# Kernel tuning notes

Measured on AMD Instinct MI355X. Metric: run time of the kernel, lower is better.

## Reference

```python
import jax, jax.numpy as jnp
import numpy as np

B, D, L = 16, 64, 1280
H = 8            # nhead
WIN = 5          # window_size (divides L exactly)
DFF = 128        # dim_feedforward
EPS = 1e-5


def _layernorm(x, g, b):
    mu = jnp.mean(x, axis=-1, keepdims=True)
    var = jnp.mean(jnp.square(x - mu), axis=-1, keepdims=True)
    return (x - mu) * jax.lax.rsqrt(var + EPS) * g + b


def _mha(x, w_in, b_in, w_out, b_out):
    # x: (Bx, Lx, D). torch nn.MultiheadAttention, batch_first, eval mode.
    Bx, Lx, Dm = x.shape
    hd = Dm // H
    qkv = x @ w_in.T + b_in                      # (Bx, Lx, 3D)
    q, k, v = jnp.split(qkv, 3, axis=-1)
    q = q.reshape(Bx, Lx, H, hd)
    k = k.reshape(Bx, Lx, H, hd)
    v = v.reshape(Bx, Lx, H, hd)
    scale = 1.0 / jnp.sqrt(jnp.asarray(hd, x.dtype))
    scores = jnp.einsum('bqhd,bkhd->bhqk', q, k) * scale
    att = jax.nn.softmax(scores, axis=-1)
    out = jnp.einsum('bhqk,bkhd->bqhd', att, v).reshape(Bx, Lx, Dm)
    return out @ w_out.T + b_out


def setup_inputs() -> dict:
    key = jax.random.key(0)
    ks = jax.random.split(key, 16)
    s = 0.05
    return {
        'x': jax.random.normal(ks[0], (B, D, L), dtype=jnp.float32),
        # local attention params
        'lw_in': jax.random.normal(ks[1], (3 * D, D), dtype=jnp.float32) * s,
        'lb_in': jnp.zeros((3 * D,), jnp.float32),
        'lw_out': jax.random.normal(ks[2], (D, D), dtype=jnp.float32) * s,
        'lb_out': jnp.zeros((D,), jnp.float32),
        # global attention params
        'gw_in': jax.random.normal(ks[3], (3 * D, D), dtype=jnp.float32) * s,
        'gb_in': jnp.zeros((3 * D,), jnp.float32),
        'gw_out': jax.random.normal(ks[4], (D, D), dtype=jnp.float32) * s,
        'gb_out': jnp.zeros((D,), jnp.float32),
        # gating weight (init 0.5 like the module)
        'local_weight': jnp.full((D,), 0.5, jnp.float32),
        # layer norms
        'g1': jnp.ones((D,), jnp.float32), 'b1': jnp.zeros((D,), jnp.float32),
        'g2': jnp.ones((D,), jnp.float32), 'b2': jnp.zeros((D,), jnp.float32),
        'g3': jnp.ones((D,), jnp.float32), 'b3': jnp.zeros((D,), jnp.float32),
        # FFN
        'w1': jax.random.normal(ks[5], (DFF, D), dtype=jnp.float32) * s,
        'bf1': jnp.zeros((DFF,), jnp.float32),
        'w2': jax.random.normal(ks[6], (D, DFF), dtype=jnp.float32) * s,
        'bf2': jnp.zeros((D,), jnp.float32),
    }


def reference(x, lw_in, lb_in, lw_out, lb_out, gw_in, gb_in, gw_out, gb_out,
              local_weight, g1, b1, g2, b2, g3, b3, w1, bf1, w2, bf2):
    xt = jnp.transpose(x, (0, 2, 1))              # (B, L, D)
    residual = xt
    nW = L // WIN
    xw = xt.reshape(B * nW, WIN, D)
    local_out = _mha(xw, lw_in, lb_in, lw_out, lb_out).reshape(B, L, D)
    local_out = _layernorm(local_out + residual, g1, b1)
    # global attention
    global_out = _mha(xt, gw_in, gb_in, gw_out, gb_out)
    global_out = _layernorm(global_out + residual, g2, b2)
    # gated channel fusion
    alpha = jax.nn.sigmoid(local_weight)[None, None, :]
    fused = alpha * local_out + (1.0 - alpha) * global_out
    # FFN (dropout is identity in eval mode)
    ffn_out = jax.nn.relu(fused @ w1.T + bf1) @ w2.T + bf2
    out = _layernorm(ffn_out + fused, g3, b3)
    return jnp.transpose(out, (0, 2, 1))          # (B, D, L)
```

## Files before the change

kernel.cpp:

```cpp
#include <hip/hip_runtime.h>
#include <math.h>

typedef short bf16x8 __attribute__((ext_vector_type(8)));
typedef float f32x4 __attribute__((ext_vector_type(4)));
typedef unsigned short u16;
typedef unsigned int u32;

#define RFL(x) __builtin_amdgcn_readfirstlane(x)

static __device__ __forceinline__ float bf2f(u16 s) {
  union { u32 u; float f; } c; c.u = ((u32)s) << 16; return c.f;
}
static __device__ __forceinline__ u16 f2bf(float f) {
  union { float f; u32 u; } c; c.f = f;
  u32 u = c.u + 0x7fffu + ((c.u >> 16) & 1u);
  return (u16)(u >> 16);
}
static __device__ __forceinline__ u32 pk2(float lo, float hi) {
  u32 r;
  asm("v_cvt_pk_bf16_f32 %0, %1, %2" : "=v"(r) : "v"(lo), "v"(hi));
  return r;
}
static __device__ __forceinline__ f32x4 MF(bf16x8 a, bf16x8 b, f32x4 c) {
  return __builtin_amdgcn_mfma_f32_16x16x32_bf16(a, b, c, 0, 0, 0);
}


__global__ __launch_bounds__(256) void prep_kernel(
    const float* __restrict__ x,
    const float* __restrict__ lw_in, const float* __restrict__ gw_in,
    const float* __restrict__ lw_out, const float* __restrict__ gw_out,
    const float* __restrict__ w1, const float* __restrict__ w2,
    u16* __restrict__ XT, u16* __restrict__ Wqkv,
    u16* __restrict__ Wlout, u16* __restrict__ Wgout,
    u16* __restrict__ W1b, u16* __restrict__ W2b) {
  const int t = threadIdx.x;
  if (blockIdx.x < 320) {
    __shared__ __align__(16) float xs[64][68];
    const int b = blockIdx.x / 20, l0 = (blockIdx.x % 20) * 64;
    for (int i = t; i < 4096; i += 256) {
      const int d = i >> 6, tok = i & 63;
      xs[tok][d] = x[(b * 64 + d) * 1280 + l0 + tok];
    }
    __syncthreads();
    for (int i = t; i < 512; i += 256) {
      const int tok = i >> 3, c8 = (i & 7) * 8;
      union { bf16x8 v; u32 u[4]; } o;
      const float* src = &xs[tok][c8];
      o.u[0] = pk2(src[0], src[1]); o.u[1] = pk2(src[2], src[3]);
      o.u[2] = pk2(src[4], src[5]); o.u[3] = pk2(src[6], src[7]);
      *(bf16x8*)(XT + (b * 1280 + l0 + tok) * 64 + c8) = o.v;
    }
  } else {
    const int wb = blockIdx.x - 320;
    for (int f = wb * 256 + t; f < 49152; f += 24 * 256) {
      if (f < 12288)      Wqkv[f] = f2bf(lw_in[f]);
      else if (f < 24576) Wqkv[f] = f2bf(gw_in[f - 12288]);
      else if (f < 28672) Wlout[f - 24576] = f2bf(lw_out[f - 24576]);
      else if (f < 32768) Wgout[f - 28672] = f2bf(gw_out[f - 28672]);
      else if (f < 40960) W1b[f - 32768] = f2bf(w1[f - 32768]);
      else                W2b[f - 40960] = f2bf(w2[f - 40960]);
    }
  }
}

__global__ __launch_bounds__(256) void qkv_gemm(
    const u16* __restrict__ XT, const u16* __restrict__ Wqkv,
    const float* __restrict__ lb_in, const float* __restrict__ gb_in,
    u16* __restrict__ QKV) {
  const int t = threadIdx.x;
  const int lane = t & 63, w = RFL(t >> 6);
  const int lr = lane & 15, lg = lane >> 4;
  const int m0 = blockIdx.x * 64 + (w & 1) * 32;
  const int n0 = blockIdx.y * 96 + (w >> 1) * 48;
  bf16x8 a[2][2], bb[3][2];
#pragma unroll
  for (int mt = 0; mt < 2; ++mt)
#pragma unroll
    for (int ks = 0; ks < 2; ++ks)
      a[mt][ks] = *(const bf16x8*)(XT + (m0 + mt * 16 + lr) * 64 + ks * 32 + lg * 8);
#pragma unroll
  for (int nt = 0; nt < 3; ++nt)
#pragma unroll
    for (int ks = 0; ks < 2; ++ks)
      bb[nt][ks] = *(const bf16x8*)(Wqkv + (n0 + nt * 16 + lr) * 64 + ks * 32 + lg * 8);
  f32x4 acc[2][3];
#pragma unroll
  for (int mt = 0; mt < 2; ++mt)
#pragma unroll
    for (int nt = 0; nt < 3; ++nt) {
      f32x4 z = {0.f, 0.f, 0.f, 0.f};
      acc[mt][nt] = z;
#pragma unroll
      for (int ks = 0; ks < 2; ++ks)
        acc[mt][nt] = MF(a[mt][ks], bb[nt][ks], acc[mt][nt]);
    }
#pragma unroll
  for (int nt = 0; nt < 3; ++nt) {
    const int col = n0 + nt * 16 + lr;
    const float bias = (col < 192) ? lb_in[col] : gb_in[col - 192];
    const float scale = (col < 64) ? 0.35355339059327373f
                      : ((col >= 192 && col < 256) ? 0.51010407600615432f : 1.f);
#pragma unroll
    for (int mt = 0; mt < 2; ++mt)
#pragma unroll
      for (int r = 0; r < 4; ++r) {
        const int row = m0 + mt * 16 + 4 * lg + r;
        QKV[row * 384 + col] = f2bf((acc[mt][nt][r] + bias) * scale);
      }
  }
}

__global__ __launch_bounds__(256) void latt(const u16* __restrict__ QKV,
                                            u16* __restrict__ AOl) {
  const int g = blockIdx.x * 256 + threadIdx.x;
  const int qi = g % 5, h = (g / 5) & 7, wi = (g / 40) & 255, b = g / 10240;
  const int row = b * 1280 + wi * 5 + qi;
  float q[8];
  {
    bf16x8 qv = *(const bf16x8*)(QKV + row * 384 + h * 8);
#pragma unroll
    for (int d = 0; d < 8; ++d) q[d] = bf2f((u16)qv[d]);
  }
  float p[5], sum = 0.f;
#pragma unroll
  for (int j = 0; j < 5; ++j) {
    const int krow = b * 1280 + wi * 5 + j;
    bf16x8 kv = *(const bf16x8*)(QKV + krow * 384 + 64 + h * 8);
    float s = 0.f;
#pragma unroll
    for (int d = 0; d < 8; ++d) s = fmaf(q[d], bf2f((u16)kv[d]), s);
    p[j] = __expf(s); sum += p[j];
  }
  const float inv = 1.f / sum;
  float o[8] = {0, 0, 0, 0, 0, 0, 0, 0};
#pragma unroll
  for (int j = 0; j < 5; ++j) {
    const int vrow = b * 1280 + wi * 5 + j;
    bf16x8 vv = *(const bf16x8*)(QKV + vrow * 384 + 128 + h * 8);
#pragma unroll
    for (int d = 0; d < 8; ++d) o[d] = fmaf(p[j], bf2f((u16)vv[d]), o[d]);
  }
  union { bf16x8 v; u32 u[4]; } ov;
  ov.u[0] = pk2(o[0] * inv, o[1] * inv); ov.u[1] = pk2(o[2] * inv, o[3] * inv);
  ov.u[2] = pk2(o[4] * inv, o[5] * inv); ov.u[3] = pk2(o[6] * inv, o[7] * inv);
  *(bf16x8*)(AOl + row * 64 + h * 8) = ov.v;
}

__global__ __launch_bounds__(512) void gatt(const u16* __restrict__ QKV,
                                            u16* __restrict__ AOg) {
  __shared__ __align__(16) u16 Klds[1280 * 8];
  __shared__ __align__(16) u16 VT[9 * 1320];
  const int t = threadIdx.x;
  const int b = blockIdx.y >> 3, h = blockIdx.y & 7;
  for (int l = t; l < 1280; l += 512) {
    const int src = (b * 1280 + l) * 384 + h * 8;
    bf16x8 kv = *(const bf16x8*)(QKV + src + 256);
    bf16x8 vv = *(const bf16x8*)(QKV + src + 320);
    const int k5 = l & 31;
    const int pos = (l & ~31) + (((k5 >> 2) & 1) << 4) + (k5 & 3) + ((k5 >> 3) << 2);
    *(bf16x8*)(Klds + pos * 8) = kv;
#pragma unroll
    for (int d = 0; d < 8; ++d) VT[d * 1320 + l] = (u16)vv[d];
  }
  for (int l = t; l < 1320; l += 512) VT[8 * 1320 + l] = 0x3F80;
  __syncthreads();
  const int lane = t & 63, w = RFL(t >> 6);
  const int c = lane & 15, lg = lane >> 4;
  const int q0 = blockIdx.x * 128 + w * 16;
  const int qrow = b * 1280 + q0 + c;
  const bf16x8 qv = *(const bf16x8*)(QKV + qrow * 384 + 192 + h * 8);
  const bf16x8 qz = {0, 0, 0, 0, 0, 0, 0, 0};
  const bf16x8 qf = (lg == 0) ? qv : qz;
  const u16* kp = Klds + c * 8;
  const int vrow = (c < 8) ? c : 8;
  const u16* vp = VT + vrow * 1320 + lg * 8;
  f32x4 oacc = {0.f, 0.f, 0.f, 0.f};
#pragma unroll 4
  for (int jt = 0; jt < 40; ++jt) {
    bf16x8 kf0 = *(const bf16x8*)kp;
    bf16x8 kf1 = *(const bf16x8*)(kp + 128);
    f32x4 z = {0.f, 0.f, 0.f, 0.f};
    f32x4 s0 = MF(kf0, qf, z);
    f32x4 s1 = MF(kf1, qf, z);
    const float p0 = __builtin_amdgcn_exp2f(s0[0]);
    const float p1 = __builtin_amdgcn_exp2f(s0[1]);
    const float p2 = __builtin_amdgcn_exp2f(s0[2]);
    const float p3 = __builtin_amdgcn_exp2f(s0[3]);
    const float p4 = __builtin_amdgcn_exp2f(s1[0]);
    const float p5 = __builtin_amdgcn_exp2f(s1[1]);
    const float p6 = __builtin_amdgcn_exp2f(s1[2]);
    const float p7 = __builtin_amdgcn_exp2f(s1[3]);
    union { u32 u[4]; bf16x8 v; } pb;
    pb.u[0] = pk2(p0, p1);
    pb.u[1] = pk2(p2, p3);
    pb.u[2] = pk2(p4, p5);
    pb.u[3] = pk2(p6, p7);
    bf16x8 vf = *(const bf16x8*)vp;
    oacc = MF(vf, pb.v, oacc);
    kp += 256; vp += 32;
  }
  const float ssum = __shfl(oacc[0], 32 + c);
  const float inv = 1.f / ssum;
  if (lg < 2) {
    const int base = qrow * 64 + h * 8 + lg * 4;
    *(u32*)(AOg + base) = pk2(oacc[0] * inv, oacc[1] * inv);
    *(u32*)(AOg + base + 2) = pk2(oacc[2] * inv, oacc[3] * inv);
  }
}

__global__ __launch_bounds__(256) void tail_kernel(
    const u16* __restrict__ AOl, const u16* __restrict__ AOg,
    const u16* __restrict__ Wlout, const u16* __restrict__ Wgout,
    const u16* __restrict__ W1b, const u16* __restrict__ W2b,
    const float* __restrict__ lb_out, const float* __restrict__ gb_out,
    const float* __restrict__ lwt,
    const float* __restrict__ g1, const float* __restrict__ b1,
    const float* __restrict__ g2, const float* __restrict__ b2,
    const float* __restrict__ g3, const float* __restrict__ b3,
    const float* __restrict__ bf1, const float* __restrict__ bf2,
    const float* __restrict__ x, float* __restrict__ out) {
  __shared__ __align__(16) float xso[64][68];
  __shared__ __align__(16) u16 Ft[64 * 64];
  __shared__ __align__(16) u16 Ht[64 * 128];
  const int t = threadIdx.x;
  const int b = blockIdx.y, l0 = blockIdx.x * 64;
  for (int i = t; i < 4096; i += 256) {
    const int d = i >> 6, tok = i & 63;
    xso[d][tok] = x[(b * 64 + d) * 1280 + l0 + tok];
  }
  __syncthreads();
  const int lane = t & 63, w = RFL(t >> 6);
  const int lr = lane & 15, lg = lane >> 4;
  const int tb = w * 16;
  const int grow = b * 1280 + l0 + tb;

  f32x4 accl[4], accg[4];
#pragma unroll
  for (int nt = 0; nt < 4; ++nt) { f32x4 z = {0,0,0,0}; accl[nt] = z; accg[nt] = z; }
#pragma unroll
  for (int ks = 0; ks < 2; ++ks) {
    bf16x8 al = *(const bf16x8*)(AOl + (grow + lr) * 64 + ks * 32 + lg * 8);
    bf16x8 ag = *(const bf16x8*)(AOg + (grow + lr) * 64 + ks * 32 + lg * 8);
#pragma unroll
    for (int nt = 0; nt < 4; ++nt) {
      bf16x8 bl = *(const bf16x8*)(Wlout + (nt * 16 + lr) * 64 + ks * 32 + lg * 8);
      bf16x8 bg = *(const bf16x8*)(Wgout + (nt * 16 + lr) * 64 + ks * 32 + lg * 8);
      accl[nt] = MF(al, bl, accl[nt]);
      accg[nt] = MF(ag, bg, accg[nt]);
    }
  }
#pragma unroll
  for (int nt = 0; nt < 4; ++nt) {
    const int col = nt * 16 + lr;
    const float bl = lb_out[col], bg = gb_out[col];
    f32x4 xr = *(const f32x4*)&xso[col][tb + lg * 4];
#pragma unroll
    for (int r = 0; r < 4; ++r) {
      accl[nt][r] += bl + xr[r];
      accg[nt][r] += bg + xr[r];
    }
  }
  auto LN = [&](f32x4* a, const float* gam, const float* bet) {
    float gv[4], bv[4];
#pragma unroll
    for (int nt = 0; nt < 4; ++nt) { gv[nt] = gam[nt * 16 + lr]; bv[nt] = bet[nt * 16 + lr]; }
#pragma unroll
    for (int r = 0; r < 4; ++r) {
      float s = a[0][r] + a[1][r] + a[2][r] + a[3][r];
      s += __shfl_xor(s, 1); s += __shfl_xor(s, 2);
      s += __shfl_xor(s, 4); s += __shfl_xor(s, 8);
      const float mu = s * 0.015625f;
      float q = 0.f;
#pragma unroll
      for (int nt = 0; nt < 4; ++nt) { const float cv = a[nt][r] - mu; q = fmaf(cv, cv, q); }
      q += __shfl_xor(q, 1); q += __shfl_xor(q, 2);
      q += __shfl_xor(q, 4); q += __shfl_xor(q, 8);
      const float rsq = rsqrtf(q * 0.015625f + 1e-5f);
#pragma unroll
      for (int nt = 0; nt < 4; ++nt)
        a[nt][r] = (a[nt][r] - mu) * rsq * gv[nt] + bv[nt];
    }
  };
  LN(accl, g1, b1);
  LN(accg, g2, b2);
  f32x4 fus[4];
#pragma unroll
  for (int nt = 0; nt < 4; ++nt) {
    const int col = nt * 16 + lr;
    const float al_ = 1.f / (1.f + __expf(-lwt[col]));
#pragma unroll
    for (int r = 0; r < 4; ++r)
      fus[nt][r] = al_ * accl[nt][r] + (1.f - al_) * accg[nt][r];
  }
#pragma unroll
  for (int nt = 0; nt < 4; ++nt)
#pragma unroll
    for (int r = 0; r < 4; ++r) {
      const int ltok = tb + lg * 4 + r;
      const int byteoff = ((ltok * 64 + nt * 16 + lr) * 2) ^ ((ltok & 7) << 4);
      *(u16*)((char*)Ft + byteoff) = f2bf(fus[nt][r]);
    }
  asm volatile("" ::: "memory");
  __syncthreads();
  f32x4 hcc[8];
#pragma unroll
  for (int nt = 0; nt < 8; ++nt) { f32x4 z = {0,0,0,0}; hcc[nt] = z; }
#pragma unroll
  for (int ks = 0; ks < 2; ++ks) {
    const int ltokA = tb + lr;
    const int abyte = (ltokA * 128 + ks * 64 + lg * 16) ^ ((ltokA & 7) << 4);
    bf16x8 af = *(const bf16x8*)((char*)Ft + abyte);
#pragma unroll
    for (int nt = 0; nt < 8; ++nt) {
      bf16x8 bw = *(const bf16x8*)(W1b + (nt * 16 + lr) * 64 + ks * 32 + lg * 8);
      hcc[nt] = MF(af, bw, hcc[nt]);
    }
  }
#pragma unroll
  for (int nt = 0; nt < 8; ++nt) {
    const int f = nt * 16 + lr;
    const float bbv = bf1[f];
#pragma unroll
    for (int r = 0; r < 4; ++r) {
      const float v = fmaxf(hcc[nt][r] + bbv, 0.f);
      const int ltok = tb + lg * 4 + r;
      const int byteoff = ((ltok * 256 + f * 2)) ^ ((ltok & 7) << 4);
      *(u16*)((char*)Ht + byteoff) = f2bf(v);
    }
  }
  asm volatile("" ::: "memory");
  f32x4 occ[4];
#pragma unroll
  for (int nt = 0; nt < 4; ++nt) { f32x4 z = {0,0,0,0}; occ[nt] = z; }
#pragma unroll
  for (int ks = 0; ks < 4; ++ks) {
    const int ltokA = tb + lr;
    const int abyte = (ltokA * 256 + ks * 64 + lg * 16) ^ ((ltokA & 7) << 4);
    bf16x8 af = *(const bf16x8*)((char*)Ht + abyte);
#pragma unroll
    for (int nt = 0; nt < 4; ++nt) {
      bf16x8 bw = *(const bf16x8*)(W2b + (nt * 16 + lr) * 128 + ks * 32 + lg * 8);
      occ[nt] = MF(af, bw, occ[nt]);
    }
  }
#pragma unroll
  for (int nt = 0; nt < 4; ++nt) {
    const float bb2 = bf2[nt * 16 + lr];
#pragma unroll
    for (int r = 0; r < 4; ++r) occ[nt][r] += bb2 + fus[nt][r];
  }
  LN(occ, g3, b3);
#pragma unroll
  for (int nt = 0; nt < 4; ++nt)
#pragma unroll
    for (int r = 0; r < 4; ++r)
      xso[nt * 16 + lr][tb + lg * 4 + r] = occ[nt][r];
  __syncthreads();
  for (int i = t; i < 4096; i += 256) {
    const int d = i >> 6, tok = i & 63;
    out[(b * 64 + d) * 1280 + l0 + tok] = xso[d][tok];
  }
}

extern "C" void kernel_launch(void* const* d_in, const int* in_sizes, int n_in,
                              void* d_out, int out_size, void* d_ws,
                              size_t ws_size, hipStream_t stream) {
  const float* x      = (const float*)d_in[0];
  const float* lw_in  = (const float*)d_in[1];
  const float* lb_in  = (const float*)d_in[2];
  const float* lw_out = (const float*)d_in[3];
  const float* lb_out = (const float*)d_in[4];
  const float* gw_in  = (const float*)d_in[5];
  const float* gb_in  = (const float*)d_in[6];
  const float* gw_out = (const float*)d_in[7];
  const float* gb_out = (const float*)d_in[8];
  const float* lwt    = (const float*)d_in[9];
  const float* g1 = (const float*)d_in[10]; const float* b1 = (const float*)d_in[11];
  const float* g2 = (const float*)d_in[12]; const float* b2 = (const float*)d_in[13];
  const float* g3 = (const float*)d_in[14]; const float* b3 = (const float*)d_in[15];
  const float* w1 = (const float*)d_in[16]; const float* bf1 = (const float*)d_in[17];
  const float* w2 = (const float*)d_in[18]; const float* bf2 = (const float*)d_in[19];
  float* out = (float*)d_out;

  u16* XT    = (u16*)d_ws;
  u16* QKV   = XT + 1310720;
  u16* AOl   = QKV + 7864320;
  u16* AOg   = AOl + 1310720;
  u16* Wqkv  = AOg + 1310720;
  u16* Wlout = Wqkv + 24576;
  u16* Wgout = Wlout + 4096;
  u16* W1b   = Wgout + 4096;
  u16* W2b   = W1b + 8192;

  dim3 blk(256);
  prep_kernel<<<dim3(344), blk, 0, stream>>>(x, lw_in, gw_in, lw_out, gw_out,
                                             w1, w2, XT, Wqkv, Wlout, Wgout, W1b, W2b);
  qkv_gemm<<<dim3(320, 4), blk, 0, stream>>>(XT, Wqkv, lb_in, gb_in, QKV);
  latt<<<dim3(640), blk, 0, stream>>>(QKV, AOl);
  gatt<<<dim3(10, 128), dim3(512), 0, stream>>>(QKV, AOg);
  tail_kernel<<<dim3(20, 16), blk, 0, stream>>>(
      AOl, AOg, Wlout, Wgout, W1b, W2b, lb_out, gb_out, lwt,
      g1, b1, g2, b2, g3, b3, bf1, bf2, x, out);
}
```

Baseline: 79.57 us.

## Fuse prep into QKV GEMM, merge attention kernels, shrink tail blocks

Fuses the x transpose/bf16 conversion and in_proj weight conversion straight into the QKV GEMM, which now stages x through swizzled LDS and converts fp32 weights in registers. The local attention, global attention and remaining weight conversion become one launch by partitioning the grid. The tail kernel moves to 64-thread blocks over 16 tokens for more blocks. Together this drops two launches and the XT/Wqkv workspace round trip, at the cost of each QKV block re-reading and re-converting the full fp32 weights, and a more heterogeneous grid in the merged attention kernel.

```diff
diff --git a/kernel.cpp b/kernel.cpp
--- a/kernel.cpp
+++ b/kernel.cpp
@@ -26,69 +26,61 @@
 }
 
 
-__global__ __launch_bounds__(256) void prep_kernel(
-    const float* __restrict__ x,
-    const float* __restrict__ lw_in, const float* __restrict__ gw_in,
-    const float* __restrict__ lw_out, const float* __restrict__ gw_out,
-    const float* __restrict__ w1, const float* __restrict__ w2,
-    u16* __restrict__ XT, u16* __restrict__ Wqkv,
-    u16* __restrict__ Wlout, u16* __restrict__ Wgout,
-    u16* __restrict__ W1b, u16* __restrict__ W2b) {
+__global__ __launch_bounds__(256) void qkvx(
+    const float* __restrict__ x, const float* __restrict__ lw_in,
+    const float* __restrict__ gw_in, const float* __restrict__ lb_in,
+    const float* __restrict__ gb_in, u16* __restrict__ QKV) {
+  __shared__ __align__(16) float xs[32][68];
+  __shared__ __align__(16) u16 XTs[32 * 64];
   const int t = threadIdx.x;
-  if (blockIdx.x < 320) {
-    __shared__ __align__(16) float xs[64][68];
-    const int b = blockIdx.x / 20, l0 = (blockIdx.x % 20) * 64;
-    for (int i = t; i < 4096; i += 256) {
-      const int d = i >> 6, tok = i & 63;
-      xs[tok][d] = x[(b * 64 + d) * 1280 + l0 + tok];
-    }
-    __syncthreads();
-    for (int i = t; i < 512; i += 256) {
-      const int tok = i >> 3, c8 = (i & 7) * 8;
-      union { bf16x8 v; u32 u[4]; } o;
-      const float* src = &xs[tok][c8];
-      o.u[0] = pk2(src[0], src[1]); o.u[1] = pk2(src[2], src[3]);
-      o.u[2] = pk2(src[4], src[5]); o.u[3] = pk2(src[6], src[7]);
-      *(bf16x8*)(XT + (b * 1280 + l0 + tok) * 64 + c8) = o.v;
-    }
-  } else {
-    const int wb = blockIdx.x - 320;
-    for (int f = wb * 256 + t; f < 49152; f += 24 * 256) {
-      if (f < 12288)      Wqkv[f] = f2bf(lw_in[f]);
-      else if (f < 24576) Wqkv[f] = f2bf(gw_in[f - 12288]);
-      else if (f < 28672) Wlout[f - 24576] = f2bf(lw_out[f - 24576]);
-      else if (f < 32768) Wgout[f - 28672] = f2bf(gw_out[f - 28672]);
-      else if (f < 40960) W1b[f - 32768] = f2bf(w1[f - 32768]);
-      else                W2b[f - 40960] = f2bf(w2[f - 40960]);
-    }
-  }
-}
-
-__global__ __launch_bounds__(256) void qkv_gemm(
-    const u16* __restrict__ XT, const u16* __restrict__ Wqkv,
-    const float* __restrict__ lb_in, const float* __restrict__ gb_in,
-    u16* __restrict__ QKV) {
-  const int t = threadIdx.x;
+  const int b = blockIdx.x / 40, l0 = (blockIdx.x % 40) * 32;
+  for (int i = t; i < 2048; i += 256) {
+    const int d = i >> 5, tok = i & 31;
+    xs[tok][d] = x[(b * 64 + d) * 1280 + l0 + tok];
+  }
+  __syncthreads();
+  {
+    const int tok = t >> 3, c8 = (t & 7) * 8;
+    union { bf16x8 v; u32 u[4]; } o;
+    const float* src = &xs[tok][c8];
+    o.u[0] = pk2(src[0], src[1]); o.u[1] = pk2(src[2], src[3]);
+    o.u[2] = pk2(src[4], src[5]); o.u[3] = pk2(src[6], src[7]);
+    const int byteoff = (tok * 128 + c8 * 2) ^ ((tok & 7) << 4);
+    *(bf16x8*)((char*)XTs + byteoff) = o.v;
+  }
+  __syncthreads();
   const int lane = t & 63, w = RFL(t >> 6);
   const int lr = lane & 15, lg = lane >> 4;
-  const int m0 = blockIdx.x * 64 + (w & 1) * 32;
-  const int n0 = blockIdx.y * 96 + (w >> 1) * 48;
-  bf16x8 a[2][2], bb[3][2];
+  const int n0 = w * 96;
+  bf16x8 a[2][2];
 #pragma unroll
   for (int mt = 0; mt < 2; ++mt)
 #pragma unroll
-    for (int ks = 0; ks < 2; ++ks)
-      a[mt][ks] = *(const bf16x8*)(XT + (m0 + mt * 16 + lr) * 64 + ks * 32 + lg * 8);
-#pragma unroll
-  for (int nt = 0; nt < 3; ++nt)
-#pragma unroll
-    for (int ks = 0; ks < 2; ++ks)
-      bb[nt][ks] = *(const bf16x8*)(Wqkv + (n0 + nt * 16 + lr) * 64 + ks * 32 + lg * 8);
-  f32x4 acc[2][3];
+    for (int ks = 0; ks < 2; ++ks) {
+      const int row = mt * 16 + lr;
+      const int abyte = (row * 128 + ks * 64 + lg * 16) ^ ((row & 7) << 4);
+      a[mt][ks] = *(const bf16x8*)((char*)XTs + abyte);
+    }
+  const float* W32 = (n0 < 192) ? lw_in : gw_in;
+  const int nb = (n0 < 192) ? n0 : n0 - 192;
+  bf16x8 bb[6][2];
+#pragma unroll
+  for (int nt = 0; nt < 6; ++nt)
+#pragma unroll
+    for (int ks = 0; ks < 2; ++ks) {
+      const float* src = W32 + (nb + nt * 16 + lr) * 64 + ks * 32 + lg * 8;
+      const float4 f0 = *(const float4*)src;
+      const float4 f1 = *(const float4*)(src + 4);
+      union { bf16x8 v; u32 u[4]; } o;
+      o.u[0] = pk2(f0.x, f0.y); o.u[1] = pk2(f0.z, f0.w);
+      o.u[2] = pk2(f1.x, f1.y); o.u[3] = pk2(f1.z, f1.w);
+      bb[nt][ks] = o.v;
+    }
+  f32x4 acc[2][6];
 #pragma unroll
   for (int mt = 0; mt < 2; ++mt)
 #pragma unroll
-    for (int nt = 0; nt < 3; ++nt) {
+    for (int nt = 0; nt < 6; ++nt) {
       f32x4 z = {0.f, 0.f, 0.f, 0.f};
       acc[mt][nt] = z;
 #pragma unroll
@@ -96,7 +88,7 @@
         acc[mt][nt] = MF(a[mt][ks], bb[nt][ks], acc[mt][nt]);
     }
 #pragma unroll
-  for (int nt = 0; nt < 3; ++nt) {
+  for (int nt = 0; nt < 6; ++nt) {
     const int col = n0 + nt * 16 + lr;
     const float bias = (col < 192) ? lb_in[col] : gb_in[col - 192];
     const float scale = (col < 64) ? 0.35355339059327373f
@@ -105,111 +97,123 @@
     for (int mt = 0; mt < 2; ++mt)
 #pragma unroll
       for (int r = 0; r < 4; ++r) {
-        const int row = m0 + mt * 16 + 4 * lg + r;
+        const int row = b * 1280 + l0 + mt * 16 + 4 * lg + r;
         QKV[row * 384 + col] = f2bf((acc[mt][nt][r] + bias) * scale);
       }
   }
 }
 
-__global__ __launch_bounds__(256) void latt(const u16* __restrict__ QKV,
-                                            u16* __restrict__ AOl) {
-  const int g = blockIdx.x * 256 + threadIdx.x;
-  const int qi = g % 5, h = (g / 5) & 7, wi = (g / 40) & 255, b = g / 10240;
-  const int row = b * 1280 + wi * 5 + qi;
-  float q[8];
-  {
-    bf16x8 qv = *(const bf16x8*)(QKV + row * 384 + h * 8);
-#pragma unroll
-    for (int d = 0; d < 8; ++d) q[d] = bf2f((u16)qv[d]);
-  }
-  float p[5], sum = 0.f;
-#pragma unroll
-  for (int j = 0; j < 5; ++j) {
-    const int krow = b * 1280 + wi * 5 + j;
-    bf16x8 kv = *(const bf16x8*)(QKV + krow * 384 + 64 + h * 8);
-    float s = 0.f;
-#pragma unroll
-    for (int d = 0; d < 8; ++d) s = fmaf(q[d], bf2f((u16)kv[d]), s);
-    p[j] = __expf(s); sum += p[j];
-  }
-  const float inv = 1.f / sum;
-  float o[8] = {0, 0, 0, 0, 0, 0, 0, 0};
-#pragma unroll
-  for (int j = 0; j < 5; ++j) {
-    const int vrow = b * 1280 + wi * 5 + j;
-    bf16x8 vv = *(const bf16x8*)(QKV + vrow * 384 + 128 + h * 8);
-#pragma unroll
-    for (int d = 0; d < 8; ++d) o[d] = fmaf(p[j], bf2f((u16)vv[d]), o[d]);
-  }
-  union { bf16x8 v; u32 u[4]; } ov;
-  ov.u[0] = pk2(o[0] * inv, o[1] * inv); ov.u[1] = pk2(o[2] * inv, o[3] * inv);
-  ov.u[2] = pk2(o[4] * inv, o[5] * inv); ov.u[3] = pk2(o[6] * inv, o[7] * inv);
-  *(bf16x8*)(AOl + row * 64 + h * 8) = ov.v;
-}
-
-__global__ __launch_bounds__(512) void gatt(const u16* __restrict__ QKV,
-                                            u16* __restrict__ AOg) {
+__global__ __launch_bounds__(512) void attn(
+    const u16* __restrict__ QKV, u16* __restrict__ AOl, u16* __restrict__ AOg,
+    const float* __restrict__ lw_out, const float* __restrict__ gw_out,
+    const float* __restrict__ w1, const float* __restrict__ w2,
+    u16* __restrict__ Wlout, u16* __restrict__ Wgout,
+    u16* __restrict__ W1b, u16* __restrict__ W2b) {
   __shared__ __align__(16) u16 Klds[1280 * 8];
   __shared__ __align__(16) u16 VT[9 * 1320];
   const int t = threadIdx.x;
-  const int b = blockIdx.y >> 3, h = blockIdx.y & 7;
-  for (int l = t; l < 1280; l += 512) {
-    const int src = (b * 1280 + l) * 384 + h * 8;
-    bf16x8 kv = *(const bf16x8*)(QKV + src + 256);
-    bf16x8 vv = *(const bf16x8*)(QKV + src + 320);
-    const int k5 = l & 31;
-    const int pos = (l & ~31) + (((k5 >> 2) & 1) << 4) + (k5 & 3) + ((k5 >> 3) << 2);
-    *(bf16x8*)(Klds + pos * 8) = kv;
-#pragma unroll
-    for (int d = 0; d < 8; ++d) VT[d * 1320 + l] = (u16)vv[d];
-  }
-  for (int l = t; l < 1320; l += 512) VT[8 * 1320 + l] = 0x3F80;
-  __syncthreads();
-  const int lane = t & 63, w = RFL(t >> 6);
-  const int c = lane & 15, lg = lane >> 4;
-  const int q0 = blockIdx.x * 128 + w * 16;
-  const int qrow = b * 1280 + q0 + c;
-  const bf16x8 qv = *(const bf16x8*)(QKV + qrow * 384 + 192 + h * 8);
-  const bf16x8 qz = {0, 0, 0, 0, 0, 0, 0, 0};
-  const bf16x8 qf = (lg == 0) ? qv : qz;
-  const u16* kp = Klds + c * 8;
-  const int vrow = (c < 8) ? c : 8;
-  const u16* vp = VT + vrow * 1320 + lg * 8;
-  f32x4 oacc = {0.f, 0.f, 0.f, 0.f};
+  if (blockIdx.x < 10) {
+    const int b = blockIdx.y >> 3, h = blockIdx.y & 7;
+    for (int l = t; l < 1280; l += 512) {
+      const int src = (b * 1280 + l) * 384 + h * 8;
+      bf16x8 kv = *(const bf16x8*)(QKV + src + 256);
+      bf16x8 vv = *(const bf16x8*)(QKV + src + 320);
+      const int k5 = l & 31;
+      const int pos = (l & ~31) + (((k5 >> 2) & 1) << 4) + (k5 & 3) + ((k5 >> 3) << 2);
+      *(bf16x8*)(Klds + pos * 8) = kv;
+#pragma unroll
+      for (int d = 0; d < 8; ++d) VT[d * 1320 + l] = (u16)vv[d];
+    }
+    for (int l = t; l < 1320; l += 512) VT[8 * 1320 + l] = 0x3F80;
+    __syncthreads();
+    const int lane = t & 63, w = RFL(t >> 6);
+    const int c = lane & 15, lg = lane >> 4;
+    const int q0 = blockIdx.x * 128 + w * 16;
+    const int qrow = b * 1280 + q0 + c;
+    const bf16x8 qv = *(const bf16x8*)(QKV + qrow * 384 + 192 + h * 8);
+    const bf16x8 qz = {0, 0, 0, 0, 0, 0, 0, 0};
+    const bf16x8 qf = (lg == 0) ? qv : qz;
+    const u16* kp = Klds + c * 8;
+    const int vrow = (c < 8) ? c : 8;
+    const u16* vp = VT + vrow * 1320 + lg * 8;
+    f32x4 oacc = {0.f, 0.f, 0.f, 0.f};
 #pragma unroll 4
-  for (int jt = 0; jt < 40; ++jt) {
-    bf16x8 kf0 = *(const bf16x8*)kp;
-    bf16x8 kf1 = *(const bf16x8*)(kp + 128);
-    f32x4 z = {0.f, 0.f, 0.f, 0.f};
-    f32x4 s0 = MF(kf0, qf, z);
-    f32x4 s1 = MF(kf1, qf, z);
-    const float p0 = __builtin_amdgcn_exp2f(s0[0]);
-    const float p1 = __builtin_amdgcn_exp2f(s0[1]);
-    const float p2 = __builtin_amdgcn_exp2f(s0[2]);
-    const float p3 = __builtin_amdgcn_exp2f(s0[3]);
-    const float p4 = __builtin_amdgcn_exp2f(s1[0]);
-    const float p5 = __builtin_amdgcn_exp2f(s1[1]);
-    const float p6 = __builtin_amdgcn_exp2f(s1[2]);
-    const float p7 = __builtin_amdgcn_exp2f(s1[3]);
-    union { u32 u[4]; bf16x8 v; } pb;
-    pb.u[0] = pk2(p0, p1);
-    pb.u[1] = pk2(p2, p3);
-    pb.u[2] = pk2(p4, p5);
-    pb.u[3] = pk2(p6, p7);
-    bf16x8 vf = *(const bf16x8*)vp;
-    oacc = MF(vf, pb.v, oacc);
-    kp += 256; vp += 32;
-  }
-  const float ssum = __shfl(oacc[0], 32 + c);
-  const float inv = 1.f / ssum;
-  if (lg < 2) {
-    const int base = qrow * 64 + h * 8 + lg * 4;
-    *(u32*)(AOg + base) = pk2(oacc[0] * inv, oacc[1] * inv);
-    *(u32*)(AOg + base + 2) = pk2(oacc[2] * inv, oacc[3] * inv);
-  }
-}
-
-__global__ __launch_bounds__(256) void tail_kernel(
+    for (int jt = 0; jt < 40; ++jt) {
+      bf16x8 kf0 = *(const bf16x8*)kp;
+      bf16x8 kf1 = *(const bf16x8*)(kp + 128);
+      f32x4 z = {0.f, 0.f, 0.f, 0.f};
+      f32x4 s0 = MF(kf0, qf, z);
+      f32x4 s1 = MF(kf1, qf, z);
+      const float p0 = __builtin_amdgcn_exp2f(s0[0]);
+      const float p1 = __builtin_amdgcn_exp2f(s0[1]);
+      const float p2 = __builtin_amdgcn_exp2f(s0[2]);
+      const float p3 = __builtin_amdgcn_exp2f(s0[3]);
+      const float p4 = __builtin_amdgcn_exp2f(s1[0]);
+      const float p5 = __builtin_amdgcn_exp2f(s1[1]);
+      const float p6 = __builtin_amdgcn_exp2f(s1[2]);
+      const float p7 = __builtin_amdgcn_exp2f(s1[3]);
+      union { u32 u[4]; bf16x8 v; } pb;
+      pb.u[0] = pk2(p0, p1);
+      pb.u[1] = pk2(p2, p3);
+      pb.u[2] = pk2(p4, p5);
+      pb.u[3] = pk2(p6, p7);
+      bf16x8 vf = *(const bf16x8*)vp;
+      oacc = MF(vf, pb.v, oacc);
+      kp += 256; vp += 32;
+    }
+    const float ssum = __shfl(oacc[0], 32 + c);
+    const float inv = 1.f / ssum;
+    if (lg < 2) {
+      const int base = qrow * 64 + h * 8 + lg * 4;
+      *(u32*)(AOg + base) = pk2(oacc[0] * inv, oacc[1] * inv);
+      *(u32*)(AOg + base + 2) = pk2(oacc[2] * inv, oacc[3] * inv);
+    }
+    return;
+  }
+  const int lid = (blockIdx.x - 10) * 128 + blockIdx.y;
+  if (lid < 320) {
+    const int g = lid * 512 + t;
+    const int qi = g % 5, h = (g / 5) & 7, wi = (g / 40) & 255, b = g / 10240;
+    const int row = b * 1280 + wi * 5 + qi;
+    float q[8];
+    {
+      bf16x8 qv = *(const bf16x8*)(QKV + row * 384 + h * 8);
+#pragma unroll
+      for (int d = 0; d < 8; ++d) q[d] = bf2f((u16)qv[d]);
+    }
+    float p[5], sum = 0.f;
+#pragma unroll
+    for (int j = 0; j < 5; ++j) {
+      const int krow = b * 1280 + wi * 5 + j;
+      bf16x8 kv = *(const bf16x8*)(QKV + krow * 384 + 64 + h * 8);
+      float s = 0.f;
+#pragma unroll
+      for (int d = 0; d < 8; ++d) s = fmaf(q[d], bf2f((u16)kv[d]), s);
+      p[j] = __expf(s); sum += p[j];
+    }
+    const float inv = 1.f / sum;
+    float o[8] = {0, 0, 0, 0, 0, 0, 0, 0};
+#pragma unroll
+    for (int j = 0; j < 5; ++j) {
+      const int vrow = b * 1280 + wi * 5 + j;
+      bf16x8 vv = *(const bf16x8*)(QKV + vrow * 384 + 128 + h * 8);
+#pragma unroll
+      for (int d = 0; d < 8; ++d) o[d] = fmaf(p[j], bf2f((u16)vv[d]), o[d]);
+    }
+    union { bf16x8 v; u32 u[4]; } ov;
+    ov.u[0] = pk2(o[0] * inv, o[1] * inv); ov.u[1] = pk2(o[2] * inv, o[3] * inv);
+    ov.u[2] = pk2(o[4] * inv, o[5] * inv); ov.u[3] = pk2(o[6] * inv, o[7] * inv);
+    *(bf16x8*)(AOl + row * 64 + h * 8) = ov.v;
+  } else {
+    const int f = (lid - 320) * 512 + t;
+    if (f < 4096)       Wlout[f] = f2bf(lw_out[f]);
+    else if (f < 8192)  Wgout[f - 4096] = f2bf(gw_out[f - 4096]);
+    else if (f < 16384) W1b[f - 8192] = f2bf(w1[f - 8192]);
+    else if (f < 24576) W2b[f - 16384] = f2bf(w2[f - 16384]);
+  }
+}
+
+__global__ __launch_bounds__(64) void tail_kernel(
     const u16* __restrict__ AOl, const u16* __restrict__ AOg,
     const u16* __restrict__ Wlout, const u16* __restrict__ Wgout,
     const u16* __restrict__ W1b, const u16* __restrict__ W2b,
@@ -220,20 +224,18 @@
     const float* __restrict__ g3, const float* __restrict__ b3,
     const float* __restrict__ bf1, const float* __restrict__ bf2,
     const float* __restrict__ x, float* __restrict__ out) {
-  __shared__ __align__(16) float xso[64][68];
-  __shared__ __align__(16) u16 Ft[64 * 64];
-  __shared__ __align__(16) u16 Ht[64 * 128];
+  __shared__ __align__(16) float xso[64][20];
+  __shared__ __align__(16) u16 Ft[16 * 64];
+  __shared__ __align__(16) u16 Ht[16 * 128];
   const int t = threadIdx.x;
-  const int b = blockIdx.y, l0 = blockIdx.x * 64;
-  for (int i = t; i < 4096; i += 256) {
-    const int d = i >> 6, tok = i & 63;
+  const int b = blockIdx.y, l0 = blockIdx.x * 16;
+  for (int i = t; i < 1024; i += 64) {
+    const int d = i >> 4, tok = i & 15;
     xso[d][tok] = x[(b * 64 + d) * 1280 + l0 + tok];
   }
   __syncthreads();
-  const int lane = t & 63, w = RFL(t >> 6);
-  const int lr = lane & 15, lg = lane >> 4;
-  const int tb = w * 16;
-  const int grow = b * 1280 + l0 + tb;
+  const int lr = t & 15, lg = (t & 63) >> 4;
+  const int grow = b * 1280 + l0;
 
   f32x4 accl[4], accg[4];
 #pragma unroll
@@ -254,7 +256,7 @@
   for (int nt = 0; nt < 4; ++nt) {
     const int col = nt * 16 + lr;
     const float bl = lb_out[col], bg = gb_out[col];
-    f32x4 xr = *(const f32x4*)&xso[col][tb + lg * 4];
+    f32x4 xr = *(const f32x4*)&xso[col][lg * 4];
 #pragma unroll
     for (int r = 0; r < 4; ++r) {
       accl[nt][r] += bl + xr[r];
@@ -297,8 +299,8 @@
   for (int nt = 0; nt < 4; ++nt)
 #pragma unroll
     for (int r = 0; r < 4; ++r) {
-      const int ltok = tb + lg * 4 + r;
-      const int byteoff = ((ltok * 64 + nt * 16 + lr) * 2) ^ ((ltok & 7) << 4);
+      const int ltok = lg * 4 + r;
+      const int byteoff = (ltok * 128 + (nt * 16 + lr) * 2) ^ ((ltok & 7) << 4);
       *(u16*)((char*)Ft + byteoff) = f2bf(fus[nt][r]);
     }
   asm volatile("" ::: "memory");
@@ -308,8 +310,7 @@
   for (int nt = 0; nt < 8; ++nt) { f32x4 z = {0,0,0,0}; hcc[nt] = z; }
 #pragma unroll
   for (int ks = 0; ks < 2; ++ks) {
-    const int ltokA = tb + lr;
-    const int abyte = (ltokA * 128 + ks * 64 + lg * 16) ^ ((ltokA & 7) << 4);
+    const int abyte = (lr * 128 + ks * 64 + lg * 16) ^ ((lr & 7) << 4);
     bf16x8 af = *(const bf16x8*)((char*)Ft + abyte);
 #pragma unroll
     for (int nt = 0; nt < 8; ++nt) {
@@ -324,8 +325,8 @@
 #pragma unroll
     for (int r = 0; r < 4; ++r) {
       const float v = fmaxf(hcc[nt][r] + bbv, 0.f);
-      const int ltok = tb + lg * 4 + r;
-      const int byteoff = ((ltok * 256 + f * 2)) ^ ((ltok & 7) << 4);
+      const int ltok = lg * 4 + r;
+      const int byteoff = (ltok * 256 + f * 2) ^ ((ltok & 7) << 4);
       *(u16*)((char*)Ht + byteoff) = f2bf(v);
     }
   }
@@ -335,8 +336,7 @@
   for (int nt = 0; nt < 4; ++nt) { f32x4 z = {0,0,0,0}; occ[nt] = z; }
 #pragma unroll
   for (int ks = 0; ks < 4; ++ks) {
-    const int ltokA = tb + lr;
-    const int abyte = (ltokA * 256 + ks * 64 + lg * 16) ^ ((ltokA & 7) << 4);
+    const int abyte = (lr * 256 + ks * 64 + lg * 16) ^ ((lr & 7) << 4);
     bf16x8 af = *(const bf16x8*)((char*)Ht + abyte);
 #pragma unroll
     for (int nt = 0; nt < 4; ++nt) {
@@ -355,10 +355,10 @@
   for (int nt = 0; nt < 4; ++nt)
 #pragma unroll
     for (int r = 0; r < 4; ++r)
-      xso[nt * 16 + lr][tb + lg * 4 + r] = occ[nt][r];
+      xso[nt * 16 + lr][lg * 4 + r] = occ[nt][r];
   __syncthreads();
-  for (int i = t; i < 4096; i += 256) {
-    const int d = i >> 6, tok = i & 63;
+  for (int i = t; i < 1024; i += 64) {
+    const int d = i >> 4, tok = i & 15;
     out[(b * 64 + d) * 1280 + l0 + tok] = xso[d][tok];
   }
 }
@@ -383,23 +383,18 @@
   const float* w2 = (const float*)d_in[18]; const float* bf2 = (const float*)d_in[19];
   float* out = (float*)d_out;
 
-  u16* XT    = (u16*)d_ws;
-  u16* QKV   = XT + 1310720;
+  u16* QKV   = (u16*)d_ws;
   u16* AOl   = QKV + 7864320;
   u16* AOg   = AOl + 1310720;
-  u16* Wqkv  = AOg + 1310720;
-  u16* Wlout = Wqkv + 24576;
+  u16* Wlout = AOg + 1310720;
   u16* Wgout = Wlout + 4096;
   u16* W1b   = Wgout + 4096;
   u16* W2b   = W1b + 8192;
 
-  dim3 blk(256);
-  prep_kernel<<<dim3(344), blk, 0, stream>>>(x, lw_in, gw_in, lw_out, gw_out,
-                                             w1, w2, XT, Wqkv, Wlout, Wgout, W1b, W2b);
-  qkv_gemm<<<dim3(320, 4), blk, 0, stream>>>(XT, Wqkv, lb_in, gb_in, QKV);
-  latt<<<dim3(640), blk, 0, stream>>>(QKV, AOl);
-  gatt<<<dim3(10, 128), dim3(512), 0, stream>>>(QKV, AOg);
-  tail_kernel<<<dim3(20, 16), blk, 0, stream>>>(
+  qkvx<<<dim3(640), dim3(256), 0, stream>>>(x, lw_in, gw_in, lb_in, gb_in, QKV);
+  attn<<<dim3(13, 128), dim3(512), 0, stream>>>(QKV, AOl, AOg, lw_out, gw_out,
+                                                w1, w2, Wlout, Wgout, W1b, W2b);
+  tail_kernel<<<dim3(80, 16), dim3(64), 0, stream>>>(
       AOl, AOg, Wlout, Wgout, W1b, W2b, lb_out, gb_out, lwt,
       g1, b1, g2, b2, g3, b3, bf1, bf2, x, out);
 }
```

After: 73.86 us. 1.08x faster.
